# Kernel tuning notes

Hardware: AMD Instinct MI355X
Metric: run time of the kernel (lower is better)

## Reference

```python
import jax, jax.numpy as jnp
import numpy as np

N, E = 50000, 500000          # nodes per type, edges per message type
F_IN, H, L = 128, 128, 8      # input feat, hidden_size, num_labels
EPS, SLOPE = 1e-5, 0.01       # BatchNorm eps, LeakyReLU slope


def setup_inputs() -> dict:
    key = jax.random.key(0)
    ks = jax.random.split(key, 16)
    s = 0.05
    d = {}
    d["x_n0"] = jax.random.normal(ks[0], (N, F_IN), jnp.float32)
    d["x_n1"] = jax.random.normal(ks[1], (N, F_IN), jnp.float32)
    # stacked per-message-type SAGE params (3 message types), two layers
    d["Wn1"] = jax.random.normal(ks[2], (3, F_IN, H), jnp.float32) * s
    d["Ws1"] = jax.random.normal(ks[3], (3, F_IN, H), jnp.float32) * s
    d["Wu1"] = jax.random.normal(ks[4], (3, 2 * H, H), jnp.float32) * s
    d["Wn2"] = jax.random.normal(ks[5], (3, H, H), jnp.float32) * s
    d["Ws2"] = jax.random.normal(ks[6], (3, H, H), jnp.float32) * s
    d["Wu2"] = jax.random.normal(ks[7], (3, 2 * H, H), jnp.float32) * s
    for nm in ("bn1", "bs1", "bu1", "bn2", "bs2", "bu2"):
        d[nm] = jnp.zeros((3, H), jnp.float32)
    # per-node-type BatchNorm affine params (2 node types), two layers
    d["gamma1"] = jnp.ones((2, H), jnp.float32)
    d["beta1"] = jnp.zeros((2, H), jnp.float32)
    d["gamma2"] = jnp.ones((2, H), jnp.float32)
    d["beta2"] = jnp.zeros((2, H), jnp.float32)
    # per-node-type post-MP linear
    d["Wp"] = jax.random.normal(ks[8], (2, H, L), jnp.float32) * s
    d["bp"] = jnp.zeros((2, L), jnp.float32)
    # edge_index per message type: [2, E] with row0=src, row1=dst
    d["ei0"] = jax.random.randint(ks[9], (2, E), 0, N, jnp.int32)   # n0 -> n1
    d["ei1"] = jax.random.randint(ks[10], (2, E), 0, N, jnp.int32)  # n1 -> n0
    d["ei2"] = jax.random.randint(ks[11], (2, E), 0, N, jnp.int32)  # n0 -> n0
    return d


def _segment_mean(x, idx, n):
    s = jax.ops.segment_sum(x, idx, num_segments=n)
    c = jax.ops.segment_sum(jnp.ones((idx.shape[0], 1), x.dtype), idx, num_segments=n)
    return s / jnp.maximum(c, 1.0)


def _sage(x_src, x_dst, ei, Wn, bn, Ws, bs, Wu, bu):
    # gather source feats per edge, scatter-mean to dst, then linear branches
    agg = _segment_mean(x_src[ei[0]], ei[1], x_dst.shape[0])  # [N_dst, F]
    h = jnp.concatenate([agg @ Wn + bn, x_dst @ Ws + bs], axis=-1)
    return h @ Wu + bu


def _bn(x, g, b):
    m = x.mean(0)
    v = ((x - m) ** 2).mean(0)  # biased variance, as torch BN training mode
    return (x - m) * jax.lax.rsqrt(v + EPS) * g + b


def _lrelu(x):
    return jnp.where(x >= 0, x, SLOPE * x)


def _layer(x0, x1, ei0, ei1, ei2, Wn, bn, Ws, bs, Wu, bu, gamma, beta):
    m0 = _sage(x0, x1, ei0, Wn[0], bn[0], Ws[0], bs[0], Wu[0], bu[0])  # dst n1
    m1 = _sage(x1, x0, ei1, Wn[1], bn[1], Ws[1], bs[1], Wu[1], bu[1])  # dst n0
    m2 = _sage(x0, x0, ei2, Wn[2], bn[2], Ws[2], bs[2], Wu[2], bu[2])  # dst n0
    h0 = 0.5 * (m1 + m2)   # mean over the 2 message types targeting n0
    h1 = m0                # single message type for n1
    h0 = _lrelu(_bn(h0, gamma[0], beta[0]))
    h1 = _lrelu(_bn(h1, gamma[1], beta[1]))
    return h0, h1


def reference(x_n0, x_n1, Wn1, bn1, Ws1, bs1, Wu1, bu1,
              Wn2, bn2, Ws2, bs2, Wu2, bu2,
              gamma1, beta1, gamma2, beta2, Wp, bp, ei0, ei1, ei2):
    h0, h1 = _layer(x_n0, x_n1, ei0, ei1, ei2, Wn1, bn1, Ws1, bs1, Wu1, bu1, gamma1, beta1)
    h0, h1 = _layer(h0, h1, ei0, ei1, ei2, Wn2, bn2, Ws2, bs2, Wu2, bu2, gamma2, beta2)
    out0 = h0 @ Wp[0] + bp[0]
    out1 = h1 @ Wp[1] + bp[1]
    return jnp.stack([out0, out1])  # [2, N, L]
```

## Files before the change

### kernel.cpp

```cpp
#include <hip/hip_runtime.h>

#define LBL 8
#define NBMAX 128
#define BSH 9
#define BCAP 8192

typedef __attribute__((ext_vector_type(8))) short short8;
typedef __attribute__((ext_vector_type(4))) float f32x4;

__device__ __forceinline__ uint f2bf(float x) {
    uint u = __float_as_uint(x);
    return (u + 0x7fffu + ((u >> 16) & 1u)) >> 16;
}
__device__ __forceinline__ float bflo(uint v) { return __uint_as_float(v << 16); }
__device__ __forceinline__ float bfhi(uint v) { return __uint_as_float(v & 0xffff0000u); }

__device__ __forceinline__ void gload16(const ushort* g, ushort* l) {
    __builtin_amdgcn_global_load_lds((const __attribute__((address_space(1))) uint*)g,
                                     (__attribute__((address_space(3))) uint*)l, 16, 0, 0);
}

__global__ void f2b2(const float4* __restrict__ x0, const float4* __restrict__ x1,
                     uint2* __restrict__ o0, uint2* __restrict__ o1, int n4) {
    int y = blockIdx.y;
    const float4* in = y ? x1 : x0;
    uint2* out = y ? o1 : o0;
    int i = blockIdx.x * blockDim.x + threadIdx.x;
    int stride = gridDim.x * blockDim.x;
    for (; i < n4; i += stride) {
        float4 v = in[i];
        uint2 o;
        o.x = f2bf(v.x) | (f2bf(v.y) << 16);
        o.y = f2bf(v.z) | (f2bf(v.w) << 16);
        out[i] = o;
    }
}


__global__ void bhist3(const int* __restrict__ e0, const int* __restrict__ e1,
                       const int* __restrict__ e2, int E, int NB, int* __restrict__ bcnt) {
    int m = blockIdx.y;
    const int* dst = (m == 0 ? e0 : (m == 1 ? e1 : e2)) + E;
    __shared__ int h[NBMAX];
    int tid = threadIdx.x;
    if (tid < NB) h[tid] = 0;
    __syncthreads();
    int i = blockIdx.x * blockDim.x + tid, st = gridDim.x * blockDim.x;
    for (; i < E; i += st) atomicAdd(&h[dst[i] >> BSH], 1);
    __syncthreads();
    if (tid < NB && h[tid]) atomicAdd(&bcnt[m * NB + tid], h[tid]);
}

__global__ void bscan(const int* __restrict__ bcnt, int* __restrict__ bso,
                      int* __restrict__ gcur, int NB) {
    int m = threadIdx.x;
    if (m >= 3) return;
    int acc = 0;
    for (int b = 0; b < NB; ++b) {
        bso[m * (NB + 1) + b] = acc;
        gcur[m * NB + b] = acc;
        acc += bcnt[m * NB + b];
    }
    bso[m * (NB + 1) + NB] = acc;
}

#define BIN_CH 16
__global__ __launch_bounds__(256) void bin3(const int* __restrict__ e0, const int* __restrict__ e1,
                                            const int* __restrict__ e2, int E, int NB,
                                            int* __restrict__ gcur, uint* __restrict__ pairs) {
    int m = blockIdx.y;
    const int* eb = (m == 0 ? e0 : (m == 1 ? e1 : e2));
    const int* src = eb;
    const int* dst = eb + E;
    uint* pp = pairs + (size_t)m * E;
    int* gc = gcur + m * NB;
    __shared__ int h[NBMAX], base[NBMAX], pos[NBMAX];
    int tid = threadIdx.x;
    if (tid < NB) { h[tid] = 0; pos[tid] = 0; }
    __syncthreads();
    int i0 = blockIdx.x * (256 * BIN_CH);
    uint pk[BIN_CH];
    int bk[BIN_CH];
    #pragma unroll
    for (int u = 0; u < BIN_CH; ++u) {
        int i = i0 + u * 256 + tid;
        bk[u] = -1;
        if (i < E) {
            int s = src[i], d = dst[i];
            bk[u] = d >> BSH;
            pk[u] = (uint)s | ((uint)(d & ((1 << BSH) - 1)) << 16);
            atomicAdd(&h[bk[u]], 1);
        }
    }
    __syncthreads();
    if (tid < NB && h[tid]) base[tid] = atomicAdd(&gc[tid], h[tid]);
    __syncthreads();
    #pragma unroll
    for (int u = 0; u < BIN_CH; ++u) {
        if (bk[u] >= 0) {
            int p = base[bk[u]] + atomicAdd(&pos[bk[u]], 1);
            pp[p] = pk[u];
        }
    }
}

__global__ __launch_bounds__(256) void csr3(const uint* __restrict__ pairs, const int* __restrict__ bso,
                                            int E, int N, int NB,
                                            int* __restrict__ offs, int* __restrict__ srcs) {
    int m = blockIdx.y, b = blockIdx.x;
    const uint* pp = pairs + (size_t)m * E;
    int gstart = bso[m * (NB + 1) + b];
    int gend = bso[m * (NB + 1) + b + 1];
    int cnt = gend - gstart;
    if (cnt > BCAP) cnt = BCAP;
    int d0 = b << BSH;
    int dcnt = N - d0;
    if (dcnt > (1 << BSH)) dcnt = 1 << BSH;

    __shared__ int hist[1 << BSH], po[1 << BSH], off0[1 << BSH];
    __shared__ int lsort[BCAP];
    __shared__ int wsum[4];
    int tid = threadIdx.x;
    hist[tid] = 0;
    hist[tid + 256] = 0;
    __syncthreads();
    for (int i = tid; i < cnt; i += 256) atomicAdd(&hist[pp[gstart + i] >> 16], 1);
    __syncthreads();
    int a = hist[2 * tid], b2 = hist[2 * tid + 1];
    int s = a + b2;
    int lane = tid & 63, w = tid >> 6;
    #pragma unroll
    for (int o = 1; o < 64; o <<= 1) {
        int v = __shfl_up(s, o, 64);
        if (lane >= o) s += v;
    }
    if (lane == 63) wsum[w] = s;
    __syncthreads();
    int wp = 0;
    #pragma unroll
    for (int q = 0; q < 4; ++q)
        if (q < w) wp += wsum[q];
    int excl = wp + s - a - b2;
    off0[2 * tid] = excl; off0[2 * tid + 1] = excl + a;
    po[2 * tid] = excl;   po[2 * tid + 1] = excl + a;
    __syncthreads();
    for (int j = tid; j < dcnt; j += 256) offs[(size_t)m * (N + 1) + d0 + j] = gstart + off0[j];
    if (b == NB - 1 && tid == 0) offs[(size_t)m * (N + 1) + N] = bso[m * (NB + 1) + NB];
    for (int i = tid; i < cnt; i += 256) {
        uint e = pp[gstart + i];
        int p = atomicAdd(&po[e >> 16], 1);
        if (p < BCAP) lsort[p] = (int)(e & 0xffffu);
    }
    __syncthreads();
    for (int i = tid; i < cnt; i += 256) srcs[(size_t)m * E + gstart + i] = lsort[i];
}

__global__ void agg3(const ushort* __restrict__ s0, const ushort* __restrict__ s1,
                     const ushort* __restrict__ s2,
                     uint* __restrict__ o0, uint* __restrict__ o1, uint* __restrict__ o2,
                     const int* __restrict__ offs, const int* __restrict__ srcs,
                     int n, int E) {
    int m = blockIdx.y;
    const uint4* x = (const uint4*)(m == 0 ? s0 : (m == 1 ? s1 : s2));
    uint4* o = (uint4*)(m == 0 ? o0 : (m == 1 ? o1 : o2));
    const int* off = offs + (size_t)m * (n + 1);
    const int* sl = srcs + (size_t)m * E;

    int tid = threadIdx.x;
    int l16 = tid & 15;
    int row = blockIdx.x * 16 + (tid >> 4);
    if (row >= n) return;
    int s = off[row], e = off[row + 1];
    float a0 = 0, a1 = 0, a2 = 0, a3 = 0, a4 = 0, a5 = 0, a6 = 0, a7 = 0;
    int i = s;
    for (; i + 3 < e; i += 4) {
        int j0 = sl[i], j1 = sl[i + 1], j2 = sl[i + 2], j3 = sl[i + 3];
        uint4 v0 = x[(size_t)j0 * 16 + l16];
        uint4 v1 = x[(size_t)j1 * 16 + l16];
        uint4 v2 = x[(size_t)j2 * 16 + l16];
        uint4 v3 = x[(size_t)j3 * 16 + l16];
        a0 += (bflo(v0.x) + bflo(v1.x)) + (bflo(v2.x) + bflo(v3.x));
        a1 += (bfhi(v0.x) + bfhi(v1.x)) + (bfhi(v2.x) + bfhi(v3.x));
        a2 += (bflo(v0.y) + bflo(v1.y)) + (bflo(v2.y) + bflo(v3.y));
        a3 += (bfhi(v0.y) + bfhi(v1.y)) + (bfhi(v2.y) + bfhi(v3.y));
        a4 += (bflo(v0.z) + bflo(v1.z)) + (bflo(v2.z) + bflo(v3.z));
        a5 += (bfhi(v0.z) + bfhi(v1.z)) + (bfhi(v2.z) + bfhi(v3.z));
        a6 += (bflo(v0.w) + bflo(v1.w)) + (bflo(v2.w) + bflo(v3.w));
        a7 += (bfhi(v0.w) + bfhi(v1.w)) + (bfhi(v2.w) + bfhi(v3.w));
    }
    for (; i < e; ++i) {
        uint4 v = x[(size_t)sl[i] * 16 + l16];
        a0 += bflo(v.x); a1 += bfhi(v.x);
        a2 += bflo(v.y); a3 += bfhi(v.y);
        a4 += bflo(v.z); a5 += bfhi(v.z);
        a6 += bflo(v.w); a7 += bfhi(v.w);
    }
    int d = e - s;
    float inv = 1.f / (float)(d > 0 ? d : 1);
    uint4 r;
    r.x = f2bf(a0 * inv) | (f2bf(a1 * inv) << 16);
    r.y = f2bf(a2 * inv) | (f2bf(a3 * inv) << 16);
    r.z = f2bf(a4 * inv) | (f2bf(a5 * inv) << 16);
    r.w = f2bf(a6 * inv) | (f2bf(a7 * inv) << 16);
    o[(size_t)row * 16 + l16] = r;
}

__global__ void fuseW(const float* __restrict__ Wn1, const float* __restrict__ Ws1,
                      const float* __restrict__ Wu1,
                      const float* __restrict__ Wn2, const float* __restrict__ Ws2,
                      const float* __restrict__ Wu2, ushort* __restrict__ FT) {
    int j5 = blockIdx.y;
    int l = j5 / 5, t = j5 - l * 5;
    const float* Wn = l ? Wn2 : Wn1;
    const float* Ws = l ? Ws2 : Ws1;
    const float* Wu = l ? Wu2 : Wu1;
    const float *A0, *B0, *A1 = nullptr, *B1 = nullptr;
    float al;
    switch (t) {
        case 0: A0 = Wn;          B0 = Wu;          al = 1.0f; break;
        case 1: A0 = Wn + 16384;  B0 = Wu + 32768;  al = 0.5f; break;
        case 2: A0 = Wn + 32768;  B0 = Wu + 65536;  al = 0.5f; break;
        case 3: A0 = Ws;          B0 = Wu + 16384;  al = 1.0f; break;
        default:
            A0 = Ws + 16384; B0 = Wu + 49152;
            A1 = Ws + 32768; B1 = Wu + 81920;
            al = 0.5f; break;
    }
    int i = blockIdx.x, j = threadIdx.x;
    float s0 = 0, s1 = 0, s2 = 0, s3 = 0;
    #pragma unroll 4
    for (int k = 0; k < 128; k += 4) {
        s0 += A0[i * 128 + k]     * B0[k * 128 + j];
        s1 += A0[i * 128 + k + 1] * B0[(k + 1) * 128 + j];
        s2 += A0[i * 128 + k + 2] * B0[(k + 2) * 128 + j];
        s3 += A0[i * 128 + k + 3] * B0[(k + 3) * 128 + j];
    }
    if (A1) {
        #pragma unroll 4
        for (int k = 0; k < 128; k += 4) {
            s0 += A1[i * 128 + k]     * B1[k * 128 + j];
            s1 += A1[i * 128 + k + 1] * B1[(k + 1) * 128 + j];
            s2 += A1[i * 128 + k + 2] * B1[(k + 2) * 128 + j];
            s3 += A1[i * 128 + k + 3] * B1[(k + 3) * 128 + j];
        }
    }
    float r = al * ((s0 + s1) + (s2 + s3));
    FT[(size_t)j5 * 16384 + j * 128 + i] = (ushort)f2bf(r);
}

__global__ void fuseB(const float* __restrict__ bn1, const float* __restrict__ bs1,
                      const float* __restrict__ bu1, const float* __restrict__ Wu1,
                      const float* __restrict__ bn2, const float* __restrict__ bs2,
                      const float* __restrict__ bu2, const float* __restrict__ Wu2,
                      float* __restrict__ FC) {
    int jb = blockIdx.x;
    int l = jb >> 1, which = jb & 1;
    const float* bn = l ? bn2 : bn1;
    const float* bs = l ? bs2 : bs1;
    const float* bu = l ? bu2 : bu1;
    const float* Wu = l ? Wu2 : Wu1;
    int j = threadIdx.x;
    float s = 0.f;
    if (which == 0) {
        s = bu[j];
        for (int k = 0; k < 128; ++k)
            s += bn[k] * Wu[k * 128 + j] + bs[k] * Wu[(128 + k) * 128 + j];
    } else {
        #pragma unroll
        for (int tt = 1; tt <= 2; ++tt) {
            const float* Wt = Wu + tt * 32768;
            float p = bu[tt * 128 + j];
            for (int k = 0; k < 128; ++k)
                p += bn[tt * 128 + k] * Wt[k * 128 + j] + bs[tt * 128 + k] * Wt[(128 + k) * 128 + j];
            s += 0.5f * p;
        }
    }
    FC[jb * 128 + j] = s;
}

__global__ __launch_bounds__(256) void gemm2_mfma(
    const ushort* __restrict__ Aq0, const ushort* __restrict__ Wq0,
    const ushort* __restrict__ Aq1, const ushort* __restrict__ Wq1,
    const ushort* __restrict__ Ap0, const ushort* __restrict__ Wp0,
    const ushort* __restrict__ Ap1, const ushort* __restrict__ Wp1,
    const ushort* __restrict__ Ap2, const ushort* __restrict__ Wp2,
    const float* __restrict__ biasq, const float* __restrict__ biasp,
    ushort* __restrict__ Cq, ushort* __restrict__ Cp, int M,
    float* __restrict__ STW) {
    __shared__ ushort As[2][64 * 128];
    int y = blockIdx.y;
    const float* bias = y ? biasp : biasq;
    ushort* C = y ? Cp : Cq;
    float* colsum = STW + (size_t)(blockIdx.x & 31) * 512 + (y ? 0 : 256);
    float* colsq = colsum + 128;

    int tid = threadIdx.x;
    int wid = tid >> 6;
    int lane = tid & 63;
    int l15 = lane & 15, lg = lane >> 4;
    int row0 = blockIdx.x * 64;
    int nIn = y ? 3 : 2;

    const ushort* Ax[3];
    const ushort* Wx[3];
    Ax[0] = y ? Ap0 : Aq0;  Wx[0] = y ? Wp0 : Wq0;
    Ax[1] = y ? Ap1 : Aq1;  Wx[1] = y ? Wp1 : Wq1;
    Ax[2] = Ap2;            Wx[2] = Wp2;

    auto stage = [&](const ushort* A, ushort* buf) {
        #pragma unroll
        for (int p = 0; p < 4; ++p) {
            int row = wid * 16 + p * 4 + (lane >> 4);
            int gr = row0 + row;
            if (gr > M - 1) gr = M - 1;
            const ushort* src = A + (size_t)gr * 128 + (((lane & 15) ^ (row & 7)) * 8);
            gload16(src, buf + (wid * 4 + p) * 512);
        }
    };

    f32x4 acc[4][2];
    #pragma unroll
    for (int rb = 0; rb < 4; ++rb)
        #pragma unroll
        for (int cb = 0; cb < 2; ++cb) acc[rb][cb] = (f32x4){0.f, 0.f, 0.f, 0.f};

    stage(Ax[0], As[0]);
    __syncthreads();
    int cur = 0;

    #pragma unroll
    for (int inp = 0; inp < 3; ++inp) {
        if (inp == 2 && nIn == 2) break;
        const ushort* W = Wx[inp];
        short8 bw[4][2];
        #pragma unroll
        for (int k0 = 0; k0 < 4; ++k0)
            #pragma unroll
            for (int cb = 0; cb < 2; ++cb)
                bw[k0][cb] = *(const short8*)(W + (size_t)(wid * 32 + cb * 16 + l15) * 128 + k0 * 32 + lg * 8);
        if (inp + 1 < nIn) stage(Ax[inp + 1], As[cur ^ 1]);
        #pragma unroll
        for (int k0 = 0; k0 < 4; ++k0) {
            short8 a[4];
            #pragma unroll
            for (int rb = 0; rb < 4; ++rb)
                a[rb] = *(const short8*)&As[cur][(rb * 16 + l15) * 128 + (((k0 * 4 + lg) ^ (l15 & 7)) * 8)];
            #pragma unroll
            for (int rb = 0; rb < 4; ++rb)
                #pragma unroll
                for (int cb = 0; cb < 2; ++cb)
                    acc[rb][cb] = __builtin_amdgcn_mfma_f32_16x16x32_bf16(a[rb], bw[k0][cb], acc[rb][cb], 0, 0, 0);
        }
        __syncthreads();
        cur ^= 1;
    }

    float ps[2] = {0.f, 0.f}, pq[2] = {0.f, 0.f};
    int colbase = wid * 32;
    #pragma unroll
    for (int cb = 0; cb < 2; ++cb) {
        int col = colbase + cb * 16 + l15;
        float b = bias[col];
        #pragma unroll
        for (int rb = 0; rb < 4; ++rb) {
            int rbase = row0 + rb * 16 + lg * 4;
            #pragma unroll
            for (int i = 0; i < 4; ++i) {
                int r = rbase + i;
                if (r < M) {
                    float v = acc[rb][cb][i] + b;
                    C[(size_t)r * 128 + col] = (ushort)f2bf(v);
                    ps[cb] += v;
                    pq[cb] += v * v;
                }
            }
        }
    }
    #pragma unroll
    for (int cb = 0; cb < 2; ++cb) {
        ps[cb] += __shfl_xor(ps[cb], 16, 64);
        ps[cb] += __shfl_xor(ps[cb], 32, 64);
        pq[cb] += __shfl_xor(pq[cb], 16, 64);
        pq[cb] += __shfl_xor(pq[cb], 32, 64);
    }
    if (lane < 16) {
        atomicAdd(&colsum[colbase + lane], ps[0]);
        atomicAdd(&colsq[colbase + lane], pq[0]);
        atomicAdd(&colsum[colbase + 16 + lane], ps[1]);
        atomicAdd(&colsq[colbase + 16 + lane], pq[1]);
    }
}

__global__ void bn_fin2(float* __restrict__ STW, float* __restrict__ ST,
                        const float* __restrict__ g0, const float* __restrict__ b0,
                        const float* __restrict__ g1, const float* __restrict__ b1, int N) {
    int tid = threadIdx.x;
    int which = tid >> 7, c = tid & 127;
    float s = 0.f, q = 0.f;
    #pragma unroll 8
    for (int cp = 0; cp < 32; ++cp) {
        s += STW[(size_t)cp * 512 + which * 256 + c];
        q += STW[(size_t)cp * 512 + which * 256 + 128 + c];
    }
    #pragma unroll 8
    for (int cp = 0; cp < 32; ++cp) {
        STW[(size_t)cp * 512 + which * 256 + c] = 0.f;
        STW[(size_t)cp * 512 + which * 256 + 128 + c] = 0.f;
    }
    const float* g = which ? g1 : g0;
    const float* b = which ? b1 : b0;
    float m = s / (float)N;
    float v = q / (float)N - m * m;
    float rs = rsqrtf(v + 1e-5f);
    float sc = g[c] * rs;
    ST[512 + which * 256 + c] = sc;
    ST[640 + which * 256 + c] = b[c] - m * sc;
}

__global__ void bn_apply2(const ushort* __restrict__ Cp, ushort* __restrict__ X0b,
                          const ushort* __restrict__ Cq, ushort* __restrict__ X1b,
                          const float* __restrict__ ST, int n4) {
    int y = blockIdx.y;
    const uint2* in = (const uint2*)(y ? Cq : Cp);
    uint2* out = (uint2*)(y ? X1b : X0b);
    const float* sc = ST + 512 + y * 256;
    const float* sh = sc + 128;
    int i = blockIdx.x * blockDim.x + threadIdx.x;
    int stride = gridDim.x * blockDim.x;
    for (; i < n4; i += stride) {
        uint2 v = in[i];
        int cb = (i * 4) & 127;
        float4 s4 = *(const float4*)&sc[cb];
        float4 h4 = *(const float4*)&sh[cb];
        float y0 = bflo(v.x) * s4.x + h4.x;
        float y1 = bfhi(v.x) * s4.y + h4.y;
        float y2 = bflo(v.y) * s4.z + h4.z;
        float y3 = bfhi(v.y) * s4.w + h4.w;
        y0 = (y0 >= 0.f) ? y0 : 0.01f * y0;
        y1 = (y1 >= 0.f) ? y1 : 0.01f * y1;
        y2 = (y2 >= 0.f) ? y2 : 0.01f * y2;
        y3 = (y3 >= 0.f) ? y3 : 0.01f * y3;
        uint2 o;
        o.x = f2bf(y0) | (f2bf(y1) << 16);
        o.y = f2bf(y2) | (f2bf(y3) << 16);
        out[i] = o;
    }
}

__global__ void projbn2(const ushort* __restrict__ Cp, const ushort* __restrict__ Cq,
                        const float* __restrict__ ST,
                        const float* __restrict__ Wp, const float* __restrict__ bp,
                        float* __restrict__ out, int N) {
    int y = blockIdx.y;
    const uint* h = (const uint*)(y ? Cq : Cp);
    const float* W = Wp + y * 1024;
    const float* b = bp + y * 8;
    float* op = out + (size_t)y * N * 8;
    __shared__ float Wsh[1024];
    __shared__ float scs[128], shs[128];
    __shared__ float bsh[8];
    int tid = threadIdx.x;
    for (int i = tid; i < 1024; i += 256) Wsh[i] = W[i];
    if (tid < 128) {
        scs[tid] = ST[512 + y * 256 + tid];
        shs[tid] = ST[640 + y * 256 + tid];
    }
    if (tid < 8) bsh[tid] = b[tid];
    __syncthreads();
    int idx = blockIdx.x * 256 + tid;
    if (idx >= N * LBL) return;
    int r = idx >> 3, c = idx & 7;
    const uint* hr = h + (size_t)r * 64;
    float s = bsh[c];
    #pragma unroll
    for (int k2 = 0; k2 < 64; ++k2) {
        uint v = hr[k2];
        float xa = bflo(v) * scs[2 * k2] + shs[2 * k2];
        float xb = bfhi(v) * scs[2 * k2 + 1] + shs[2 * k2 + 1];
        xa = (xa >= 0.f) ? xa : 0.01f * xa;
        xb = (xb >= 0.f) ? xb : 0.01f * xb;
        s += xa * Wsh[(2 * k2) * 8 + c] + xb * Wsh[(2 * k2 + 1) * 8 + c];
    }
    op[idx] = s;
}


extern "C" void kernel_launch(void* const* d_in, const int* in_sizes, int n_in,
                              void* d_out, int out_size, void* d_ws, size_t ws_size,
                              hipStream_t stream) {
    const float* x0 = (const float*)d_in[0];
    const float* x1 = (const float*)d_in[1];
    const float* Wn1 = (const float*)d_in[2];
    const float* Ws1 = (const float*)d_in[3];
    const float* Wu1 = (const float*)d_in[4];
    const float* Wn2 = (const float*)d_in[5];
    const float* Ws2 = (const float*)d_in[6];
    const float* Wu2 = (const float*)d_in[7];
    const float* bnn[2] = {(const float*)d_in[8], (const float*)d_in[11]};
    const float* bss[2] = {(const float*)d_in[9], (const float*)d_in[12]};
    const float* buu[2] = {(const float*)d_in[10], (const float*)d_in[13]};
    const float* gam[2] = {(const float*)d_in[14], (const float*)d_in[16]};
    const float* bet[2] = {(const float*)d_in[15], (const float*)d_in[17]};
    const float* Wp = (const float*)d_in[18];
    const float* bp = (const float*)d_in[19];
    const int* ei[3] = {(const int*)d_in[20], (const int*)d_in[21], (const int*)d_in[22]};

    const int N = in_sizes[0] / 128;
    const int E = in_sizes[20] / 2;
    const int NB = (N + (1 << BSH) - 1) >> BSH;
    float* out = (float*)d_out;

    char* wp_ = (char*)d_ws;
    auto carve = [&](size_t bytes) {
        char* r = wp_;
        wp_ += (bytes + 255) & ~(size_t)255;
        return r;
    };
    size_t nodeB = (size_t)N * 128 * sizeof(ushort);
    ushort* Cp = (ushort*)carve(nodeB);
    ushort* Cq = (ushort*)carve(nodeB);
    ushort* Pb = (ushort*)carve(nodeB);
    ushort* Rb = (ushort*)carve(nodeB);
    ushort* Sb = (ushort*)carve(nodeB);
    ushort* X0b = (ushort*)carve(nodeB);
    ushort* X1b = (ushort*)carve(nodeB);
    ushort* x0b = (ushort*)carve(nodeB);
    ushort* x1b = (ushort*)carve(nodeB);
    ushort* FT = (ushort*)carve(10 * 16384 * 2);
    float* FC = (float*)carve(4 * 128 * 4);
    float* ST = (float*)carve(1024 * 4);
    float* STW = (float*)carve(32 * 512 * 4);
    int* offs = (int*)carve((size_t)3 * (N + 1) * 4);
    int* srcs = (int*)carve((size_t)3 * E * 4);
    int* bcnt = (int*)carve((size_t)3 * NB * 4);
    int* bso = (int*)carve((size_t)3 * (NB + 1) * 4);
    int* gcur = (int*)carve((size_t)3 * NB * 4);
    uint* pairs = (uint*)Cp;

    const int ag = (N + 15) / 16;
    const int gg = (N + 63) / 64;
    const int pg = (N * LBL + 255) / 256;
    const int bg = (E + 256 * BIN_CH - 1) / (256 * BIN_CH);

    f2b2<<<dim3(1024, 2), 256, 0, stream>>>((const float4*)x0, (const float4*)x1,
                                            (uint2*)x0b, (uint2*)x1b, N * 32);

    hipMemsetAsync(bcnt, 0, (size_t)3 * NB * 4, stream);
    hipMemsetAsync(STW, 0, 32 * 512 * 4, stream);
    bhist3<<<dim3(512, 3), 256, 0, stream>>>(ei[0], ei[1], ei[2], E, NB, bcnt);
    bscan<<<1, 64, 0, stream>>>(bcnt, bso, gcur, NB);
    bin3<<<dim3(bg, 3), 256, 0, stream>>>(ei[0], ei[1], ei[2], E, NB, gcur, pairs);
    csr3<<<dim3(NB, 3), 256, 0, stream>>>(pairs, bso, E, N, NB, offs, srcs);

    fuseW<<<dim3(128, 10), 128, 0, stream>>>(Wn1, Ws1, Wu1, Wn2, Ws2, Wu2, FT);
    fuseB<<<4, 128, 0, stream>>>(bnn[0], bss[0], buu[0], Wu1, bnn[1], bss[1], buu[1], Wu2, FC);

    const ushort* srcS[2][3] = {{x0b, x1b, x0b}, {X0b, X1b, X0b}};
    const ushort* dstX[2][2] = {{x0b, x1b}, {X0b, X1b}};

    for (int l = 0; l < 2; ++l) {
        const ushort* FA0T = FT + (size_t)(l * 5 + 0) * 16384;
        const ushort* FA1T = FT + (size_t)(l * 5 + 1) * 16384;
        const ushort* FA2T = FT + (size_t)(l * 5 + 2) * 16384;
        const ushort* FB1T = FT + (size_t)(l * 5 + 3) * 16384;
        const ushort* FB0T = FT + (size_t)(l * 5 + 4) * 16384;
        const float* fcH1 = FC + (l * 2 + 0) * 128;
        const float* fcH0 = FC + (l * 2 + 1) * 128;

        agg3<<<dim3(ag, 3), 256, 0, stream>>>(srcS[l][0], srcS[l][1], srcS[l][2],
                                              (uint*)Pb, (uint*)Rb, (uint*)Sb,
                                              offs, srcs, N, E);

        gemm2_mfma<<<dim3(gg, 2), 256, 0, stream>>>(
            Pb, FA0T, dstX[l][1], FB1T,
            Rb, FA1T, Sb, FA2T, dstX[l][0], FB0T,
            fcH1, fcH0, Cq, Cp, N, STW);

        bn_fin2<<<1, 256, 0, stream>>>(STW, ST, gam[l], bet[l], gam[l] + 128, bet[l] + 128, N);
        if (l == 0)
            bn_apply2<<<dim3(1024, 2), 256, 0, stream>>>(Cp, X0b, Cq, X1b, ST, N * 32);
    }

    projbn2<<<dim3(pg, 2), 256, 0, stream>>>(Cp, Cq, ST, Wp, bp, out, N);
}
```

Baseline: 309.2 us.

## Sort destination rows by in-degree to balance aggregation wavefronts

Adds a degree histogram, scan and fill pass that builds a per-message-type permutation of destination nodes grouped by in-degree. The aggregation kernel then processes rows in that order, so the 16-lane groups inside a wavefront see similar edge counts and spend less time idle on divergent loop trip counts. The cost is three extra small kernels plus a memset, and the aggregation writes land in scattered rows instead of contiguous ones.

```diff
diff --git a/kernel.cpp b/kernel.cpp
--- a/kernel.cpp
+++ b/kernel.cpp
@@ -4,6 +4,7 @@
 #define NBMAX 128
 #define BSH 9
 #define BCAP 8192
+#define DBMAX 64
 
 typedef __attribute__((ext_vector_type(8))) short short8;
 typedef __attribute__((ext_vector_type(4))) float f32x4;
@@ -155,21 +156,84 @@
     for (int i = tid; i < cnt; i += 256) srcs[(size_t)m * E + gstart + i] = lsort[i];
 }
 
+__global__ void dhist3(const int* __restrict__ offs, int* __restrict__ dcnt, int N) {
+    int m = blockIdx.y;
+    const int* off = offs + (size_t)m * (N + 1);
+    __shared__ int h[DBMAX];
+    int tid = threadIdx.x;
+    if (tid < DBMAX) h[tid] = 0;
+    __syncthreads();
+    int i = blockIdx.x * blockDim.x + tid, st = gridDim.x * blockDim.x;
+    for (; i < N; i += st) {
+        int d = off[i + 1] - off[i];
+        atomicAdd(&h[d < DBMAX ? d : DBMAX - 1], 1);
+    }
+    __syncthreads();
+    if (tid < DBMAX && h[tid]) atomicAdd(&dcnt[m * DBMAX + tid], h[tid]);
+}
+
+__global__ void dscan(const int* __restrict__ dcnt, int* __restrict__ dcur) {
+    int m = threadIdx.x;
+    if (m >= 3) return;
+    int acc = 0;
+    for (int b = 0; b < DBMAX; ++b) {
+        dcur[m * DBMAX + b] = acc;
+        acc += dcnt[m * DBMAX + b];
+    }
+}
+
+#define DF_CH 8
+__global__ __launch_bounds__(256) void dfill3(const int* __restrict__ offs, int* __restrict__ dcur,
+                                              int* __restrict__ perm, int N) {
+    int m = blockIdx.y;
+    const int* off = offs + (size_t)m * (N + 1);
+    int* dc = dcur + m * DBMAX;
+    int* pm = perm + (size_t)m * N;
+    __shared__ int h[DBMAX], base[DBMAX], pos[DBMAX];
+    int tid = threadIdx.x;
+    if (tid < DBMAX) { h[tid] = 0; pos[tid] = 0; }
+    __syncthreads();
+    int i0 = blockIdx.x * (256 * DF_CH);
+    int bk[DF_CH];
+    #pragma unroll
+    for (int u = 0; u < DF_CH; ++u) {
+        int i = i0 + u * 256 + tid;
+        bk[u] = -1;
+        if (i < N) {
+            int d = off[i + 1] - off[i];
+            bk[u] = d < DBMAX ? d : DBMAX - 1;
+            atomicAdd(&h[bk[u]], 1);
+        }
+    }
+    __syncthreads();
+    if (tid < DBMAX && h[tid]) base[tid] = atomicAdd(&dc[tid], h[tid]);
+    __syncthreads();
+    #pragma unroll
+    for (int u = 0; u < DF_CH; ++u) {
+        if (bk[u] >= 0) {
+            int p = base[bk[u]] + atomicAdd(&pos[bk[u]], 1);
+            pm[p] = i0 + u * 256 + tid;
+        }
+    }
+}
+
 __global__ void agg3(const ushort* __restrict__ s0, const ushort* __restrict__ s1,
                      const ushort* __restrict__ s2,
                      uint* __restrict__ o0, uint* __restrict__ o1, uint* __restrict__ o2,
                      const int* __restrict__ offs, const int* __restrict__ srcs,
-                     int n, int E) {
+                     const int* __restrict__ perm, int n, int E) {
     int m = blockIdx.y;
     const uint4* x = (const uint4*)(m == 0 ? s0 : (m == 1 ? s1 : s2));
     uint4* o = (uint4*)(m == 0 ? o0 : (m == 1 ? o1 : o2));
     const int* off = offs + (size_t)m * (n + 1);
     const int* sl = srcs + (size_t)m * E;
+    const int* pm = perm + (size_t)m * n;
 
     int tid = threadIdx.x;
     int l16 = tid & 15;
-    int row = blockIdx.x * 16 + (tid >> 4);
-    if (row >= n) return;
+    int gid = blockIdx.x * 16 + (tid >> 4);
+    if (gid >= n) return;
+    int row = pm[gid];
     int s = off[row], e = off[row + 1];
     float a0 = 0, a1 = 0, a2 = 0, a3 = 0, a4 = 0, a5 = 0, a6 = 0, a7 = 0;
     int i = s;
@@ -532,25 +596,34 @@
     float* STW = (float*)carve(32 * 512 * 4);
     int* offs = (int*)carve((size_t)3 * (N + 1) * 4);
     int* srcs = (int*)carve((size_t)3 * E * 4);
+    int* perm = (int*)carve((size_t)3 * N * 4);
     int* bcnt = (int*)carve((size_t)3 * NB * 4);
     int* bso = (int*)carve((size_t)3 * (NB + 1) * 4);
     int* gcur = (int*)carve((size_t)3 * NB * 4);
+    int* dcnt = (int*)carve((size_t)3 * DBMAX * 4);
+    int* dcur = (int*)carve((size_t)3 * DBMAX * 4);
     uint* pairs = (uint*)Cp;
 
     const int ag = (N + 15) / 16;
     const int gg = (N + 63) / 64;
     const int pg = (N * LBL + 255) / 256;
     const int bg = (E + 256 * BIN_CH - 1) / (256 * BIN_CH);
+    const int dg = (N + 256 * DF_CH - 1) / (256 * DF_CH);
 
     f2b2<<<dim3(1024, 2), 256, 0, stream>>>((const float4*)x0, (const float4*)x1,
                                             (uint2*)x0b, (uint2*)x1b, N * 32);
 
     hipMemsetAsync(bcnt, 0, (size_t)3 * NB * 4, stream);
+    hipMemsetAsync(dcnt, 0, (size_t)3 * DBMAX * 4, stream);
     hipMemsetAsync(STW, 0, 32 * 512 * 4, stream);
     bhist3<<<dim3(512, 3), 256, 0, stream>>>(ei[0], ei[1], ei[2], E, NB, bcnt);
     bscan<<<1, 64, 0, stream>>>(bcnt, bso, gcur, NB);
     bin3<<<dim3(bg, 3), 256, 0, stream>>>(ei[0], ei[1], ei[2], E, NB, gcur, pairs);
     csr3<<<dim3(NB, 3), 256, 0, stream>>>(pairs, bso, E, N, NB, offs, srcs);
+
+    dhist3<<<dim3(64, 3), 256, 0, stream>>>(offs, dcnt, N);
+    dscan<<<1, 64, 0, stream>>>(dcnt, dcur);
+    dfill3<<<dim3(dg, 3), 256, 0, stream>>>(offs, dcur, perm, N);
 
     fuseW<<<dim3(128, 10), 128, 0, stream>>>(Wn1, Ws1, Wu1, Wn2, Ws2, Wu2, FT);
     fuseB<<<4, 128, 0, stream>>>(bnn[0], bss[0], buu[0], Wu1, bnn[1], bss[1], buu[1], Wu2, FC);
@@ -569,7 +642,7 @@
 
         agg3<<<dim3(ag, 3), 256, 0, stream>>>(srcS[l][0], srcS[l][1], srcS[l][2],
                                               (uint*)Pb, (uint*)Rb, (uint*)Sb,
-                                              offs, srcs, N, E);
+                                              offs, srcs, perm, N, E);
 
         gemm2_mfma<<<dim3(gg, 2), 256, 0, stream>>>(
             Pb, FA0T, dstX[l][1], FB1T,
```

Measured after the change: 325.6 us. +5.3%, slower.

## Sort rows by degree within windows for aggregation balance; shrink source indices to 16-bit

Applied to the files above, without the earlier changes.

Adds a kernel that buckets destination nodes by in-degree inside 1024-node windows and builds a permutation. The aggregation kernel then processes rows in that order, so the 16-lane groups within a wave get similar edge counts and spend less time diverged. Source indices in the CSR are also stored as ushort instead of int, which halves index traffic. The cost is one extra kernel launch and an extra indirection per row. Permuted row order may also reduce locality on output writes.

```diff
diff --git a/kernel.cpp b/kernel.cpp
--- a/kernel.cpp
+++ b/kernel.cpp
@@ -4,6 +4,8 @@
 #define NBMAX 128
 #define BSH 9
 #define BCAP 8192
+#define DBMAX 64
+#define WIN 1024
 
 typedef __attribute__((ext_vector_type(8))) short short8;
 typedef __attribute__((ext_vector_type(4))) float f32x4;
@@ -106,7 +108,7 @@
 
 __global__ __launch_bounds__(256) void csr3(const uint* __restrict__ pairs, const int* __restrict__ bso,
                                             int E, int N, int NB,
-                                            int* __restrict__ offs, int* __restrict__ srcs) {
+                                            int* __restrict__ offs, ushort* __restrict__ srcs) {
     int m = blockIdx.y, b = blockIdx.x;
     const uint* pp = pairs + (size_t)m * E;
     int gstart = bso[m * (NB + 1) + b];
@@ -152,24 +154,64 @@
         if (p < BCAP) lsort[p] = (int)(e & 0xffffu);
     }
     __syncthreads();
-    for (int i = tid; i < cnt; i += 256) srcs[(size_t)m * E + gstart + i] = lsort[i];
+    for (int i = tid; i < cnt; i += 256) srcs[(size_t)m * E + gstart + i] = (ushort)lsort[i];
+}
+
+__global__ __launch_bounds__(256) void wsort3(const int* __restrict__ offs,
+                                              int* __restrict__ perm, int N) {
+    int m = blockIdx.y;
+    const int* off = offs + (size_t)m * (N + 1);
+    int* pm = perm + (size_t)m * N;
+    int w0 = blockIdx.x * WIN;
+    int cnt = N - w0;
+    if (cnt > WIN) cnt = WIN;
+    __shared__ int h[DBMAX];
+    __shared__ int base[DBMAX];
+    __shared__ ushort deg[WIN];
+    int tid = threadIdx.x;
+    if (tid < DBMAX) h[tid] = 0;
+    __syncthreads();
+    for (int i = tid; i < cnt; i += 256) {
+        int d = off[w0 + i + 1] - off[w0 + i];
+        if (d >= DBMAX) d = DBMAX - 1;
+        deg[i] = (ushort)d;
+        atomicAdd(&h[d], 1);
+    }
+    __syncthreads();
+    if (tid < 64) {
+        int v = h[tid];
+        int s = v;
+        #pragma unroll
+        for (int o = 1; o < 64; o <<= 1) {
+            int t = __shfl_up(s, o, 64);
+            if (tid >= o) s += t;
+        }
+        base[tid] = s - v;
+    }
+    __syncthreads();
+    for (int i = tid; i < cnt; i += 256) {
+        int p = atomicAdd(&base[deg[i]], 1);
+        pm[w0 + p] = w0 + i;
+    }
 }
 
 __global__ void agg3(const ushort* __restrict__ s0, const ushort* __restrict__ s1,
                      const ushort* __restrict__ s2,
                      uint* __restrict__ o0, uint* __restrict__ o1, uint* __restrict__ o2,
-                     const int* __restrict__ offs, const int* __restrict__ srcs,
-                     int n, int E) {
+                     const int* __restrict__ offs, const ushort* __restrict__ srcs,
+                     const int* __restrict__ perm, int n, int E) {
     int m = blockIdx.y;
     const uint4* x = (const uint4*)(m == 0 ? s0 : (m == 1 ? s1 : s2));
     uint4* o = (uint4*)(m == 0 ? o0 : (m == 1 ? o1 : o2));
     const int* off = offs + (size_t)m * (n + 1);
-    const int* sl = srcs + (size_t)m * E;
+    const ushort* sl = srcs + (size_t)m * E;
+    const int* pm = perm + (size_t)m * n;
 
     int tid = threadIdx.x;
     int l16 = tid & 15;
-    int row = blockIdx.x * 16 + (tid >> 4);
-    if (row >= n) return;
+    int gid = blockIdx.x * 16 + (tid >> 4);
+    if (gid >= n) return;
+    int row = pm[gid];
     int s = off[row], e = off[row + 1];
     float a0 = 0, a1 = 0, a2 = 0, a3 = 0, a4 = 0, a5 = 0, a6 = 0, a7 = 0;
     int i = s;
@@ -531,7 +573,8 @@
     float* ST = (float*)carve(1024 * 4);
     float* STW = (float*)carve(32 * 512 * 4);
     int* offs = (int*)carve((size_t)3 * (N + 1) * 4);
-    int* srcs = (int*)carve((size_t)3 * E * 4);
+    ushort* srcs = (ushort*)carve((size_t)3 * E * 2);
+    int* perm = (int*)carve((size_t)3 * N * 4);
     int* bcnt = (int*)carve((size_t)3 * NB * 4);
     int* bso = (int*)carve((size_t)3 * (NB + 1) * 4);
     int* gcur = (int*)carve((size_t)3 * NB * 4);
@@ -541,6 +584,7 @@
     const int gg = (N + 63) / 64;
     const int pg = (N * LBL + 255) / 256;
     const int bg = (E + 256 * BIN_CH - 1) / (256 * BIN_CH);
+    const int wg = (N + WIN - 1) / WIN;
 
     f2b2<<<dim3(1024, 2), 256, 0, stream>>>((const float4*)x0, (const float4*)x1,
                                             (uint2*)x0b, (uint2*)x1b, N * 32);
@@ -551,6 +595,8 @@
     bscan<<<1, 64, 0, stream>>>(bcnt, bso, gcur, NB);
     bin3<<<dim3(bg, 3), 256, 0, stream>>>(ei[0], ei[1], ei[2], E, NB, gcur, pairs);
     csr3<<<dim3(NB, 3), 256, 0, stream>>>(pairs, bso, E, N, NB, offs, srcs);
+
+    wsort3<<<dim3(wg, 3), 256, 0, stream>>>(offs, perm, N);
 
     fuseW<<<dim3(128, 10), 128, 0, stream>>>(Wn1, Ws1, Wu1, Wn2, Ws2, Wu2, FT);
     fuseB<<<4, 128, 0, stream>>>(bnn[0], bss[0], buu[0], Wu1, bnn[1], bss[1], buu[1], Wu2, FC);
@@ -569,7 +615,7 @@
 
         agg3<<<dim3(ag, 3), 256, 0, stream>>>(srcS[l][0], srcS[l][1], srcS[l][2],
                                               (uint*)Pb, (uint*)Rb, (uint*)Sb,
-                                              offs, srcs, N, E);
+                                              offs, srcs, perm, N, E);
 
         gemm2_mfma<<<dim3(gg, 2), 256, 0, stream>>>(
             Pb, FA0T, dstX[l][1], FB1T,
```

New measurement: 316.8 us. 1.02x slower.
